# Optimization experiments

Hardware: AMD Instinct MI355X
Metric: run time of the kernel (lower is better)

Reference implementation:

```python
import jax, jax.numpy as jnp
import numpy as np

EPS = 1e-9
NUM_HEADS = 16
D = 1024      # input_dim == hidden_dim
B, S = 2, 2048


def layer_norm(x, scale, shift):
    mu = x.mean(axis=-1, keepdims=True)
    # torch std is unbiased (ddof=1); eps added to std, not variance
    std = jnp.std(x, axis=-1, ddof=1, keepdims=True)
    return scale * (x - mu) / (std + EPS) + shift


def setup_inputs() -> dict:
    key = jax.random.key(0)
    ks = jax.random.split(key, 18)
    d, h = D, D
    w = lambda k, sh: jax.random.normal(k, sh, dtype=jnp.float32) * 0.02
    return {
        "inputs": jax.random.normal(ks[0], (B, S, d), dtype=jnp.float32),
        "ln1_scale": jax.random.normal(ks[1], (d,), dtype=jnp.float32),
        "ln1_shift": jax.random.normal(ks[2], (d,), dtype=jnp.float32),
        "Wq": w(ks[3], (d, h)), "bq": jnp.zeros((h,), jnp.float32),
        "Wk": w(ks[4], (d, h)), "bk": jnp.zeros((h,), jnp.float32),
        "Wv": w(ks[5], (d, h)), "bv": jnp.zeros((h,), jnp.float32),
        "Wo": w(ks[6], (h, d)), "bo": jnp.zeros((d,), jnp.float32),
        "W1": w(ks[7], (d, 4 * d)), "b1": jnp.zeros((4 * d,), jnp.float32),
        "W2": w(ks[8], (4 * d, d)), "b2": jnp.zeros((d,), jnp.float32),
        "ln2_scale": jax.random.normal(ks[9], (d,), dtype=jnp.float32),
        "ln2_shift": jax.random.normal(ks[10], (d,), dtype=jnp.float32),
    }


def mhsa(x, Wq, bq, Wk, bk, Wv, bv, Wo, bo):
    b, s, d = x.shape
    nh, dh = NUM_HEADS, D // NUM_HEADS
    q = (x @ Wq + bq).reshape(b, s, nh, dh).transpose(0, 2, 1, 3)  # b h s d
    k = (x @ Wk + bk).reshape(b, s, nh, dh).transpose(0, 2, 1, 3)
    v = (x @ Wv + bv).reshape(b, s, nh, dh).transpose(0, 2, 1, 3)
    scores = jnp.einsum("bhqd,bhkd->bhqk", q, k) / jnp.sqrt(jnp.float32(dh))
    causal = jnp.triu(jnp.ones((s, s), dtype=bool), k=1)  # mask above diagonal
    scores = jnp.where(causal, -jnp.inf, scores)
    p = jax.nn.softmax(scores, axis=-1)
    p = jnp.where(jnp.isnan(p), 0.0, p)  # NaN-fill as in original
    out = jnp.einsum("bhqk,bhkd->bhqd", p, v)
    out = out.transpose(0, 2, 1, 3).reshape(b, s, nh * dh)
    return out @ Wo + bo


def reference(inputs, ln1_scale, ln1_shift, Wq, bq, Wk, bk, Wv, bv, Wo, bo,
              W1, b1, W2, b2, ln2_scale, ln2_shift):
    o1 = layer_norm(inputs, ln1_scale, ln1_shift)
    o1 = mhsa(o1, Wq, bq, Wk, bk, Wv, bv, Wo, bo) + inputs
    o2 = layer_norm(o1, ln2_scale, ln2_shift)
    # NOTE: original adds the residual from the *normalized* tensor, not o1
    ffn = jax.nn.relu(o2 @ W1 + b1) @ W2 + b2
    return ffn + o2
```

## Files before the change

### kernel.cpp

```cpp
#include <hip/hip_runtime.h>
#include <hip/hip_bf16.h>
#include <math.h>

#define BB 2
#define SS 2048
#define DD 1024
#define HH 16
#define DH 64
#define NROW (BB*SS)
#define FFN (4*DD)

typedef __attribute__((ext_vector_type(8))) __bf16 bf16x8;
typedef __attribute__((ext_vector_type(4))) float f32x4;

__device__ __forceinline__ ushort f2b(float f) {
    union { float f; uint32_t u; } x; x.f = f;
    uint32_t r = x.u + 0x7FFF + ((x.u >> 16) & 1);
    return (ushort)(r >> 16);
}
__device__ __forceinline__ float b2f(ushort u) {
    union { uint32_t u; float f; } x; x.u = (uint32_t)u << 16;
    return x.f;
}

__global__ __launch_bounds__(256)
void ln_kernel(const float* __restrict__ x, const float* __restrict__ scale,
               const float* __restrict__ shift, ushort* __restrict__ y) {
    int row = blockIdx.x;
    const float* xr = x + (size_t)row * DD;
    ushort* yr = y + (size_t)row * DD;
    int t = threadIdx.x;
    float v[4];
    float s = 0.f, ss = 0.f;
#pragma unroll
    for (int i = 0; i < 4; ++i) {
        v[i] = xr[t + 256 * i];
        s += v[i];
        ss += v[i] * v[i];
    }
#pragma unroll
    for (int off = 32; off; off >>= 1) {
        s  += __shfl_xor(s, off);
        ss += __shfl_xor(ss, off);
    }
    __shared__ float red[8];
    int w = t >> 6;
    if ((t & 63) == 0) { red[w] = s; red[w + 4] = ss; }
    __syncthreads();
    float st  = red[0] + red[1] + red[2] + red[3];
    float sst = red[4] + red[5] + red[6] + red[7];
    float mu = st * (1.f / DD);
    float var = (sst - DD * mu * mu) * (1.f / (DD - 1));
    var = fmaxf(var, 0.f);
    float inv = 1.f / (sqrtf(var) + 1e-9f);
#pragma unroll
    for (int i = 0; i < 4; ++i) {
        int c = t + 256 * i;
        yr[c] = f2b(scale[c] * (v[i] - mu) * inv + shift[c]);
    }
}

__global__ __launch_bounds__(256)
void ln_res_kernel(const ushort* __restrict__ xa, const float* __restrict__ xb,
                   const float* __restrict__ scale, const float* __restrict__ shift,
                   ushort* __restrict__ yb) {
    int row = blockIdx.x;
    const ushort* ar = xa + (size_t)row * DD;
    const float* br = xb + (size_t)row * DD;
    ushort* ybr = yb + (size_t)row * DD;
    int t = threadIdx.x;
    float v[4];
    float s = 0.f, ss = 0.f;
#pragma unroll
    for (int i = 0; i < 4; ++i) {
        int c = t + 256 * i;
        v[i] = b2f(ar[c]) + br[c];
        s += v[i];
        ss += v[i] * v[i];
    }
#pragma unroll
    for (int off = 32; off; off >>= 1) {
        s  += __shfl_xor(s, off);
        ss += __shfl_xor(ss, off);
    }
    __shared__ float red[8];
    int w = t >> 6;
    if ((t & 63) == 0) { red[w] = s; red[w + 4] = ss; }
    __syncthreads();
    float st  = red[0] + red[1] + red[2] + red[3];
    float sst = red[4] + red[5] + red[6] + red[7];
    float mu = st * (1.f / DD);
    float var = (sst - DD * mu * mu) * (1.f / (DD - 1));
    var = fmaxf(var, 0.f);
    float inv = 1.f / (sqrtf(var) + 1e-9f);
#pragma unroll
    for (int i = 0; i < 4; ++i) {
        int c = t + 256 * i;
        ybr[c] = f2b(scale[c] * (v[i] - mu) * inv + shift[c]);
    }
}

__global__ __launch_bounds__(256)
void transpose_bf16_kernel(const float* __restrict__ W, ushort* __restrict__ Wt,
                           int K, int N) {
    __shared__ ushort tile[32][33];
    int tx = threadIdx.x & 31;
    int ty = threadIdx.x >> 5;
    int n0 = blockIdx.x * 32;
    int k0 = blockIdx.y * 32;
#pragma unroll
    for (int i = 0; i < 32; i += 8)
        tile[ty + i][tx] = f2b(W[(size_t)(k0 + ty + i) * N + n0 + tx]);
    __syncthreads();
#pragma unroll
    for (int i = 0; i < 32; i += 8)
        Wt[(size_t)(n0 + ty + i) * K + k0 + tx] = tile[tx][ty + i];
}

#define GBM 128
#define GBN 128
#define GBK 32

template <int MODE, bool BF16_OUT, int DEPTH>
__global__ __launch_bounds__(512)
void gemm_bf16_kernel(const ushort* __restrict__ A, const ushort* __restrict__ Wt,
                      const float* __restrict__ bias, const ushort* __restrict__ addsrc,
                      void* __restrict__ Cout, int M, int N, int K,
                      const float* __restrict__ bias2, const float* __restrict__ bias3,
                      void* __restrict__ out2, void* __restrict__ out3) {
    __shared__ ushort As[DEPTH][GBM * GBK];
    __shared__ ushort Bs[DEPTH][GBN * GBK];

    int tid = threadIdx.x;
    int lane = tid & 63;
    int wid = tid >> 6;
    int wr = wid >> 2, wc = wid & 3;

    int gx = gridDim.x;
    int nwg = gx * gridDim.y;
    int orig = blockIdx.y * gx + blockIdx.x;
    int q8 = nwg >> 3;
    int swz = (orig & 7) * q8 + (orig >> 3);
    int bx = swz % gx, by = swz / gx;

    int brow = by * GBM;
    int bcol = bx * GBN;

    int lrow = lane & 15;
    int kgrp = lane >> 4;

    f32x4 acc[4][2] = {};

    int srow = tid >> 2;
    int sgran = (tid & 3) ^ ((srow >> 1) & 3);

    auto stage = [&](int buf, int k0) {
        const char* ga = (const char*)A +
            ((size_t)(brow + srow) * K + k0) * 2 + sgran * 16;
        __builtin_amdgcn_global_load_lds(
            (const __attribute__((address_space(1))) uint32_t*)ga,
            (__attribute__((address_space(3))) uint32_t*)(&As[buf][0] + (wid * 16) * GBK),
            16, 0, 0);
        const char* gb = (const char*)Wt +
            ((size_t)(bcol + srow) * K + k0) * 2 + sgran * 16;
        __builtin_amdgcn_global_load_lds(
            (const __attribute__((address_space(1))) uint32_t*)gb,
            (__attribute__((address_space(3))) uint32_t*)(&Bs[buf][0] + (wid * 16) * GBK),
            16, 0, 0);
    };

    int nk = K / GBK;
    constexpr int PRE = DEPTH - 1;
#pragma unroll
    for (int s = 0; s < PRE; ++s)
        if (s < nk) stage(s, s * GBK);

    int cur = 0, stg = PRE;
    for (int t = 0; t < nk; ++t) {
        __builtin_amdgcn_sched_barrier(0);
        int rem = nk - 1 - t;
        if constexpr (DEPTH == 5) {
            if (rem >= 3)      asm volatile("s_waitcnt vmcnt(6)" ::: "memory");
            else if (rem == 2) asm volatile("s_waitcnt vmcnt(4)" ::: "memory");
            else if (rem == 1) asm volatile("s_waitcnt vmcnt(2)" ::: "memory");
            else               asm volatile("s_waitcnt vmcnt(0)" ::: "memory");
        } else {
            if (rem >= 1)      asm volatile("s_waitcnt vmcnt(2)" ::: "memory");
            else               asm volatile("s_waitcnt vmcnt(0)" ::: "memory");
        }
        asm volatile("s_barrier" ::: "memory");
        if (t + PRE < nk) stage(stg, (t + PRE) * GBK);

        bf16x8 afrag[4], bfrag[2];
#pragma unroll
        for (int mi = 0; mi < 4; ++mi) {
            int row = wr * 64 + mi * 16 + lrow;
            int gran = kgrp ^ ((row >> 1) & 3);
            afrag[mi] = *(const bf16x8*)((const char*)&As[cur][0] + row * 64 + gran * 16);
        }
#pragma unroll
        for (int ni = 0; ni < 2; ++ni) {
            int row = wc * 32 + ni * 16 + lrow;
            int gran = kgrp ^ ((row >> 1) & 3);
            bfrag[ni] = *(const bf16x8*)((const char*)&Bs[cur][0] + row * 64 + gran * 16);
        }
#pragma unroll
        for (int mi = 0; mi < 4; ++mi)
#pragma unroll
            for (int ni = 0; ni < 2; ++ni)
                acc[mi][ni] = __builtin_amdgcn_mfma_f32_16x16x32_bf16(
                    afrag[mi], bfrag[ni], acc[mi][ni], 0, 0, 0);

        cur = (cur == DEPTH - 1) ? 0 : cur + 1;
        stg = (stg == DEPTH - 1) ? 0 : stg + 1;
    }

    if (MODE == 3) {
        int which = bcol >> 10;
        const float* bs = which == 0 ? bias : (which == 1 ? bias2 : bias3);
#pragma unroll
        for (int ni = 0; ni < 2; ++ni) {
            int col = bcol + wc * 32 + ni * 16 + lrow;
            int lcol = col & 1023;
            float bsv = bs[lcol];
#pragma unroll
            for (int mi = 0; mi < 4; ++mi) {
                f32x4 a = acc[mi][ni];
#pragma unroll
                for (int j = 0; j < 4; ++j) {
                    int row = brow + wr * 64 + mi * 16 + kgrp * 4 + j;
                    float val = a[j] + bsv;
                    if (which == 2) {
                        size_t idx = (size_t)(row >> 11) * ((size_t)DD * SS)
                                   + (size_t)lcol * SS + (row & (SS - 1));
                        ((ushort*)out3)[idx] = f2b(val);
                    } else {
                        ushort* dst = which == 0 ? (ushort*)Cout : (ushort*)out2;
                        dst[(size_t)row * DD + lcol] = f2b(val);
                    }
                }
            }
        }
        return;
    }

#pragma unroll
    for (int ni = 0; ni < 2; ++ni) {
        int col = bcol + wc * 32 + ni * 16 + lrow;
        float bsv = bias[col];
#pragma unroll
        for (int mi = 0; mi < 4; ++mi) {
            f32x4 a = acc[mi][ni];
#pragma unroll
            for (int j = 0; j < 4; ++j) {
                int row = brow + wr * 64 + mi * 16 + kgrp * 4 + j;
                float val = a[j] + bsv;
                if (MODE == 1) val = fmaxf(val, 0.f);
                if (MODE == 2) val += b2f(addsrc[(size_t)row * N + col]);
                if (BF16_OUT)
                    ((ushort*)Cout)[(size_t)row * N + col] = f2b(val);
                else
                    ((float*)Cout)[(size_t)row * N + col] = val;
            }
        }
    }
}

__global__ __launch_bounds__(256)
void attn_mfma_kernel(const ushort* __restrict__ Qg, const ushort* __restrict__ Kg,
                      const ushort* __restrict__ Vtg, ushort* __restrict__ Og) {
    __shared__ ushort Qs[64 * 64];
    __shared__ ushort Ks[3][64 * 64];
    __shared__ ushort Vs[3][64 * 64];
    __shared__ ushort Ps[64 * 64];

    int tid = threadIdx.x;
    int lane = tid & 63;
    int wid = tid >> 6;
    int bh = blockIdx.x;
    int b = bh >> 4, h = bh & 15;
    int q0 = ((int)gridDim.y - 1 - (int)blockIdx.y) * 64;

    const ushort* Qbase = Qg + ((size_t)(b * SS + q0)) * DD + h * DH;
    const ushort* Kbase = Kg + ((size_t)(b * SS)) * DD + h * DH;
    const ushort* Vbase = Vtg + (size_t)bh * DH * SS;

    int r0 = wid * 16;
    int rr0 = r0 + (lane >> 3);
    int g0 = lane & 7;

    auto stageKV = [&](int buf, int k0) {
#pragma unroll
        for (int i = 0; i < 2; ++i) {
            int rr = rr0 + i * 8;
            int g = g0 ^ (rr & 7);
            const ushort* srck = Kbase + (size_t)(k0 + rr) * DD + g * 8;
            __builtin_amdgcn_global_load_lds(
                (const __attribute__((address_space(1))) uint32_t*)srck,
                (__attribute__((address_space(3))) uint32_t*)(&Ks[buf][0] + (r0 + i * 8) * 64),
                16, 0, 0);
            const ushort* srcv = Vbase + (size_t)rr * SS + k0 + g * 8;
            __builtin_amdgcn_global_load_lds(
                (const __attribute__((address_space(1))) uint32_t*)srcv,
                (__attribute__((address_space(3))) uint32_t*)(&Vs[buf][0] + (r0 + i * 8) * 64),
                16, 0, 0);
        }
    };

    int nt = q0 / 64 + 1;

    {
#pragma unroll
        for (int i = 0; i < 2; ++i) {
            int rr = rr0 + i * 8;
            int g = g0 ^ (rr & 7);
            const ushort* src = Qbase + (size_t)rr * DD + g * 8;
            __builtin_amdgcn_global_load_lds(
                (const __attribute__((address_space(1))) uint32_t*)src,
                (__attribute__((address_space(3))) uint32_t*)(Qs + (r0 + i * 8) * 64),
                16, 0, 0);
        }
    }
    stageKV(0, 0);
    if (nt > 1) stageKV(1, 64);
    __builtin_amdgcn_sched_barrier(0);
    if (nt > 1) asm volatile("s_waitcnt vmcnt(8)" ::: "memory");
    else        asm volatile("s_waitcnt vmcnt(4)" ::: "memory");
    asm volatile("s_barrier" ::: "memory");

    bf16x8 aq[2];
    {
        int r = wid * 16 + (lane & 15);
#pragma unroll
        for (int ks = 0; ks < 2; ++ks) {
            int lg = ks * 4 + (lane >> 4);
            aq[ks] = *(const bf16x8*)((const char*)Qs + r * 128 + ((lg ^ (r & 7)) << 4));
        }
    }

    f32x4 oacc[4] = {};
    float m[4] = {-INFINITY, -INFINITY, -INFINITY, -INFINITY};
    float l[4] = {0.f, 0.f, 0.f, 0.f};

    int cur = 0, stg = 2;
    for (int t = 0; t < nt; ++t) {
        __builtin_amdgcn_sched_barrier(0);
        if (t + 1 < nt) asm volatile("s_waitcnt vmcnt(4)" ::: "memory");
        else            asm volatile("s_waitcnt vmcnt(0)" ::: "memory");
        asm volatile("s_barrier" ::: "memory");
        if (t + 2 < nt) stageKV(stg, (t + 2) * 64);
        int k0 = t * 64;

        f32x4 sacc[4] = {};
#pragma unroll
        for (int ni = 0; ni < 4; ++ni) {
            int r = ni * 16 + (lane & 15);
#pragma unroll
            for (int ks = 0; ks < 2; ++ks) {
                int lg = ks * 4 + (lane >> 4);
                bf16x8 bk = *(const bf16x8*)((const char*)&Ks[cur][0] + r * 128 + ((lg ^ (r & 7)) << 4));
                sacc[ni] = __builtin_amdgcn_mfma_f32_16x16x32_bf16(aq[ks], bk, sacc[ni], 0, 0, 0);
            }
        }

        float sc[4][4];
#pragma unroll
        for (int ni = 0; ni < 4; ++ni)
#pragma unroll
            for (int j = 0; j < 4; ++j)
                sc[ni][j] = sacc[ni][j] * 0.125f;
        if (k0 == q0) {
            int rl = wid * 16 + ((lane >> 4) << 2);
#pragma unroll
            for (int ni = 0; ni < 4; ++ni) {
                int key = ni * 16 + (lane & 15);
#pragma unroll
                for (int j = 0; j < 4; ++j)
                    if (key > rl + j) sc[ni][j] = -INFINITY;
            }
        }

        float p[4][4];
#pragma unroll
        for (int j = 0; j < 4; ++j) {
            float mx = fmaxf(fmaxf(sc[0][j], sc[1][j]), fmaxf(sc[2][j], sc[3][j]));
#pragma unroll
            for (int off = 1; off < 16; off <<= 1) mx = fmaxf(mx, __shfl_xor(mx, off));
            float mn = fmaxf(m[j], mx);
            float corr = __expf(m[j] - mn);
            m[j] = mn;
            float rs = 0.f;
#pragma unroll
            for (int ni = 0; ni < 4; ++ni) { p[ni][j] = __expf(sc[ni][j] - mn); rs += p[ni][j]; }
#pragma unroll
            for (int off = 1; off < 16; off <<= 1) rs += __shfl_xor(rs, off);
            l[j] = l[j] * corr + rs;
#pragma unroll
            for (int ni = 0; ni < 4; ++ni) oacc[ni][j] *= corr;
        }

        {
            int rbase = wid * 16 + ((lane >> 4) << 2);
            int cl = lane & 15;
#pragma unroll
            for (int ni = 0; ni < 4; ++ni) {
                int c = ni * 16 + cl;
                int gsh = (c >> 3);
                int blo = (c & 7) * 2;
#pragma unroll
                for (int j = 0; j < 4; ++j) {
                    int rl = rbase + j;
                    *(ushort*)((char*)Ps + rl * 128 + ((gsh ^ (rl & 7)) << 4) + blo) = f2b(p[ni][j]);
                }
            }
        }
        asm volatile("s_waitcnt lgkmcnt(0)" ::: "memory");

        bf16x8 ap[2];
        {
            int r = wid * 16 + (lane & 15);
#pragma unroll
            for (int ks = 0; ks < 2; ++ks) {
                int lg = ks * 4 + (lane >> 4);
                ap[ks] = *(const bf16x8*)((const char*)Ps + r * 128 + ((lg ^ (r & 7)) << 4));
            }
        }
#pragma unroll
        for (int ni = 0; ni < 4; ++ni) {
            int r = ni * 16 + (lane & 15);
#pragma unroll
            for (int ks = 0; ks < 2; ++ks) {
                int lg = ks * 4 + (lane >> 4);
                bf16x8 bv = *(const bf16x8*)((const char*)&Vs[cur][0] + r * 128 + ((lg ^ (r & 7)) << 4));
                oacc[ni] = __builtin_amdgcn_mfma_f32_16x16x32_bf16(ap[ks], bv, oacc[ni], 0, 0, 0);
            }
        }
        cur = (cur == 2) ? 0 : cur + 1;
        stg = (stg == 2) ? 0 : stg + 1;
    }

#pragma unroll
    for (int j = 0; j < 4; ++j) {
        float inv = 1.f / l[j];
        int gr = q0 + wid * 16 + ((lane >> 4) << 2) + j;
#pragma unroll
        for (int ni = 0; ni < 4; ++ni) {
            int d = ni * 16 + (lane & 15);
            Og[((size_t)(b * SS + gr)) * DD + h * DH + d] = f2b(oacc[ni][j] * inv);
        }
    }
}

extern "C" void kernel_launch(void* const* d_in, const int* in_sizes, int n_in,
                              void* d_out, int out_size, void* d_ws, size_t ws_size,
                              hipStream_t stream) {
    const float* inputs    = (const float*)d_in[0];
    const float* ln1_scale = (const float*)d_in[1];
    const float* ln1_shift = (const float*)d_in[2];
    const float* Wq = (const float*)d_in[3];
    const float* bq = (const float*)d_in[4];
    const float* Wk = (const float*)d_in[5];
    const float* bk = (const float*)d_in[6];
    const float* Wv = (const float*)d_in[7];
    const float* bv = (const float*)d_in[8];
    const float* Wo = (const float*)d_in[9];
    const float* bo = (const float*)d_in[10];
    const float* W1 = (const float*)d_in[11];
    const float* b1 = (const float*)d_in[12];
    const float* W2 = (const float*)d_in[13];
    const float* b2 = (const float*)d_in[14];
    const float* ln2_scale = (const float*)d_in[15];
    const float* ln2_shift = (const float*)d_in[16];
    float* out = (float*)d_out;

    const size_t MB = 1024 * 1024;
    char* w = (char*)d_ws;
    ushort* q_b   = (ushort*)(w + 0 * MB);
    ushort* k_b   = (ushort*)(w + 8 * MB);
    ushort* vt_b  = (ushort*)(w + 16 * MB);
    ushort* att_b = (ushort*)(w + 24 * MB);
    ushort* proj_b= (ushort*)(w + 32 * MB);
    ushort* o2_b  = (ushort*)(w + 48 * MB);
    ushort* h1_b  = (ushort*)(w + 64 * MB);
    ushort* wq_t  = (ushort*)(w + 96 * MB);
    ushort* wk_t  = (ushort*)(w + 98 * MB);
    ushort* wv_t  = (ushort*)(w + 100 * MB);
    ushort* wo_t  = (ushort*)(w + 102 * MB);
    ushort* w1_t  = (ushort*)(w + 104 * MB);
    ushort* w2_t  = (ushort*)(w + 112 * MB);
    ushort* xn_b  = (ushort*)(w + 120 * MB);

    transpose_bf16_kernel<<<dim3(DD / 32, DD / 32), 256, 0, stream>>>(Wq, wq_t, DD, DD);
    transpose_bf16_kernel<<<dim3(DD / 32, DD / 32), 256, 0, stream>>>(Wk, wk_t, DD, DD);
    transpose_bf16_kernel<<<dim3(DD / 32, DD / 32), 256, 0, stream>>>(Wv, wv_t, DD, DD);
    transpose_bf16_kernel<<<dim3(DD / 32, DD / 32), 256, 0, stream>>>(Wo, wo_t, DD, DD);
    transpose_bf16_kernel<<<dim3(FFN / 32, DD / 32), 256, 0, stream>>>(W1, w1_t, DD, FFN);
    transpose_bf16_kernel<<<dim3(DD / 32, FFN / 32), 256, 0, stream>>>(W2, w2_t, FFN, DD);

    ln_kernel<<<NROW, 256, 0, stream>>>(inputs, ln1_scale, ln1_shift, xn_b);

    dim3 gqkv(3 * DD / GBN, NROW / GBM);
    gemm_bf16_kernel<3, true, 3><<<gqkv, 512, 0, stream>>>(
        xn_b, wq_t, bq, nullptr, q_b, NROW, 3 * DD, DD, bk, bv, k_b, vt_b);

    dim3 ga(BB * HH, SS / 64);
    attn_mfma_kernel<<<ga, 256, 0, stream>>>(q_b, k_b, vt_b, att_b);

    dim3 g1(DD / GBN, NROW / GBM);
    gemm_bf16_kernel<0, true, 5><<<g1, 512, 0, stream>>>(
        att_b, wo_t, bo, nullptr, proj_b, NROW, DD, DD, nullptr, nullptr, nullptr, nullptr);

    ln_res_kernel<<<NROW, 256, 0, stream>>>(proj_b, inputs, ln2_scale, ln2_shift, o2_b);

    dim3 g2(FFN / GBN, NROW / GBM);
    gemm_bf16_kernel<1, true, 3><<<g2, 512, 0, stream>>>(
        o2_b, w1_t, b1, nullptr, h1_b, NROW, FFN, DD, nullptr, nullptr, nullptr, nullptr);

    gemm_bf16_kernel<2, false, 5><<<g1, 512, 0, stream>>>(
        h1_b, w2_t, b2, o2_b, out, NROW, DD, FFN, nullptr, nullptr, nullptr, nullptr);
}
```

Before: 283.3 us.

## Transpose score MFMA so each lane owns one query row in attention softmax

```diff
diff --git a/kernel.cpp b/kernel.cpp
--- a/kernel.cpp
+++ b/kernel.cpp
@@ -270,9 +270,8 @@
 void attn_mfma_kernel(const ushort* __restrict__ Qg, const ushort* __restrict__ Kg,
                       const ushort* __restrict__ Vtg, ushort* __restrict__ Og) {
     __shared__ ushort Qs[64 * 64];
-    __shared__ ushort Ks[3][64 * 64];
-    __shared__ ushort Vs[3][64 * 64];
-    __shared__ ushort Ps[64 * 64];
+    __shared__ ushort Ks[2][64 * 64];
+    __shared__ ushort Vs[2][64 * 64];
 
     int tid = threadIdx.x;
     int lane = tid & 63;
@@ -288,18 +287,20 @@
     int r0 = wid * 16;
     int rr0 = r0 + (lane >> 3);
     int g0 = lane & 7;
+    int g = lane >> 4;
+    int lr = lane & 15;
 
     auto stageKV = [&](int buf, int k0) {
 #pragma unroll
         for (int i = 0; i < 2; ++i) {
             int rr = rr0 + i * 8;
-            int g = g0 ^ (rr & 7);
-            const ushort* srck = Kbase + (size_t)(k0 + rr) * DD + g * 8;
+            int gg = g0 ^ (rr & 7);
+            const ushort* srck = Kbase + (size_t)(k0 + rr) * DD + gg * 8;
             __builtin_amdgcn_global_load_lds(
                 (const __attribute__((address_space(1))) uint32_t*)srck,
                 (__attribute__((address_space(3))) uint32_t*)(&Ks[buf][0] + (r0 + i * 8) * 64),
                 16, 0, 0);
-            const ushort* srcv = Vbase + (size_t)rr * SS + k0 + g * 8;
+            const ushort* srcv = Vbase + (size_t)rr * SS + k0 + gg * 8;
             __builtin_amdgcn_global_load_lds(
                 (const __attribute__((address_space(1))) uint32_t*)srcv,
                 (__attribute__((address_space(3))) uint32_t*)(&Vs[buf][0] + (r0 + i * 8) * 64),
@@ -313,8 +314,8 @@
 #pragma unroll
         for (int i = 0; i < 2; ++i) {
             int rr = rr0 + i * 8;
-            int g = g0 ^ (rr & 7);
-            const ushort* src = Qbase + (size_t)rr * DD + g * 8;
+            int gg = g0 ^ (rr & 7);
+            const ushort* src = Qbase + (size_t)rr * DD + gg * 8;
             __builtin_amdgcn_global_load_lds(
                 (const __attribute__((address_space(1))) uint32_t*)src,
                 (__attribute__((address_space(3))) uint32_t*)(Qs + (r0 + i * 8) * 64),
@@ -322,46 +323,44 @@
         }
     }
     stageKV(0, 0);
-    if (nt > 1) stageKV(1, 64);
-    __builtin_amdgcn_sched_barrier(0);
-    if (nt > 1) asm volatile("s_waitcnt vmcnt(8)" ::: "memory");
-    else        asm volatile("s_waitcnt vmcnt(4)" ::: "memory");
-    asm volatile("s_barrier" ::: "memory");
+    asm volatile("s_waitcnt vmcnt(4)" ::: "memory");
 
     bf16x8 aq[2];
     {
-        int r = wid * 16 + (lane & 15);
+        int r = wid * 16 + lr;
 #pragma unroll
         for (int ks = 0; ks < 2; ++ks) {
-            int lg = ks * 4 + (lane >> 4);
+            int lg = ks * 4 + g;
             aq[ks] = *(const bf16x8*)((const char*)Qs + r * 128 + ((lg ^ (r & 7)) << 4));
         }
     }
+    ushort* Ps = Qs;
 
     f32x4 oacc[4] = {};
-    float m[4] = {-INFINITY, -INFINITY, -INFINITY, -INFINITY};
-    float l[4] = {0.f, 0.f, 0.f, 0.f};
-
-    int cur = 0, stg = 2;
+    float m = -INFINITY, l = 0.f;
+    int qa = q0 + wid * 16 + lr;
+
+    int cur = 0;
     for (int t = 0; t < nt; ++t) {
         __builtin_amdgcn_sched_barrier(0);
-        if (t + 1 < nt) asm volatile("s_waitcnt vmcnt(4)" ::: "memory");
-        else            asm volatile("s_waitcnt vmcnt(0)" ::: "memory");
+        asm volatile("s_waitcnt vmcnt(0)" ::: "memory");
         asm volatile("s_barrier" ::: "memory");
-        if (t + 2 < nt) stageKV(stg, (t + 2) * 64);
+        if (t + 1 < nt) stageKV(cur ^ 1, (t + 1) * 64);
         int k0 = t * 64;
 
         f32x4 sacc[4] = {};
+        __builtin_amdgcn_s_setprio(1);
 #pragma unroll
         for (int ni = 0; ni < 4; ++ni) {
-            int r = ni * 16 + (lane & 15);
+            int r = ni * 16 + lr;
 #pragma unroll
             for (int ks = 0; ks < 2; ++ks) {
-                int lg = ks * 4 + (lane >> 4);
+                int lg = ks * 4 + g;
                 bf16x8 bk = *(const bf16x8*)((const char*)&Ks[cur][0] + r * 128 + ((lg ^ (r & 7)) << 4));
-                sacc[ni] = __builtin_amdgcn_mfma_f32_16x16x32_bf16(aq[ks], bk, sacc[ni], 0, 0, 0);
-            }
-        }
+                sacc[ni] = __builtin_amdgcn_mfma_f32_16x16x32_bf16(bk, aq[ks], sacc[ni], 0, 0, 0);
+            }
+        }
+        __builtin_amdgcn_s_setprio(0);
 
         float sc[4][4];
 #pragma unroll
@@ -370,82 +369,90 @@
             for (int j = 0; j < 4; ++j)
                 sc[ni][j] = sacc[ni][j] * 0.125f;
         if (k0 == q0) {
-            int rl = wid * 16 + ((lane >> 4) << 2);
 #pragma unroll
             for (int ni = 0; ni < 4; ++ni) {
-                int key = ni * 16 + (lane & 15);
-#pragma unroll
-                for (int j = 0; j < 4; ++j)
-                    if (key > rl + j) sc[ni][j] = -INFINITY;
-            }
-        }
-
+#pragma unroll
+                for (int j = 0; j < 4; ++j) {
+                    int key = q0 + ni * 16 + g * 4 + j;
+                    if (key > qa) sc[ni][j] = -INFINITY;
+                }
+            }
+        }
+
+        float mx = sc[0][0];
+#pragma unroll
+        for (int ni = 0; ni < 4; ++ni)
+#pragma unroll
+            for (int j = 0; j < 4; ++j) mx = fmaxf(mx, sc[ni][j]);
+        mx = fmaxf(mx, __shfl_xor(mx, 16));
+        mx = fmaxf(mx, __shfl_xor(mx, 32));
+        float mn = fmaxf(m, mx);
+        float corr = __expf(m - mn);
+        m = mn;
         float p[4][4];
-#pragma unroll
-        for (int j = 0; j < 4; ++j) {
-            float mx = fmaxf(fmaxf(sc[0][j], sc[1][j]), fmaxf(sc[2][j], sc[3][j]));
-#pragma unroll
-            for (int off = 1; off < 16; off <<= 1) mx = fmaxf(mx, __shfl_xor(mx, off));
-            float mn = fmaxf(m[j], mx);
-            float corr = __expf(m[j] - mn);
-            m[j] = mn;
-            float rs = 0.f;
-#pragma unroll
-            for (int ni = 0; ni < 4; ++ni) { p[ni][j] = __expf(sc[ni][j] - mn); rs += p[ni][j]; }
-#pragma unroll
-            for (int off = 1; off < 16; off <<= 1) rs += __shfl_xor(rs, off);
-            l[j] = l[j] * corr + rs;
-#pragma unroll
-            for (int ni = 0; ni < 4; ++ni) oacc[ni][j] *= corr;
-        }
+        float rs = 0.f;
+#pragma unroll
+        for (int ni = 0; ni < 4; ++ni)
+#pragma unroll
+            for (int j = 0; j < 4; ++j) { p[ni][j] = __expf(sc[ni][j] - mn); rs += p[ni][j]; }
+        rs += __shfl_xor(rs, 16);
+        rs += __shfl_xor(rs, 32);
+        l = l * corr + rs;
+
+        float cj[4];
+#pragma unroll
+        for (int j = 0; j < 4; ++j)
+            cj[j] = __shfl(corr, (lane & 48) | (g * 4 + j));
+#pragma unroll
+        for (int ni = 0; ni < 4; ++ni)
+#pragma unroll
+            for (int j = 0; j < 4; ++j) oacc[ni][j] *= cj[j];
 
         {
-            int rbase = wid * 16 + ((lane >> 4) << 2);
-            int cl = lane & 15;
+            int row = wid * 16 + lr;
 #pragma unroll
             for (int ni = 0; ni < 4; ++ni) {
-                int c = ni * 16 + cl;
-                int gsh = (c >> 3);
-                int blo = (c & 7) * 2;
-#pragma unroll
-                for (int j = 0; j < 4; ++j) {
-                    int rl = rbase + j;
-                    *(ushort*)((char*)Ps + rl * 128 + ((gsh ^ (rl & 7)) << 4) + blo) = f2b(p[ni][j]);
-                }
+                ushort4 w4;
+                w4.x = f2b(p[ni][0]); w4.y = f2b(p[ni][1]);
+                w4.z = f2b(p[ni][2]); w4.w = f2b(p[ni][3]);
+                int gran = (ni * 2 + (g >> 1)) ^ (row & 7);
+                *(ushort4*)((char*)Ps + row * 128 + (gran << 4) + (g & 1) * 8) = w4;
             }
         }
         asm volatile("s_waitcnt lgkmcnt(0)" ::: "memory");
 
         bf16x8 ap[2];
         {
-            int r = wid * 16 + (lane & 15);
+            int r = wid * 16 + lr;
 #pragma unroll
             for (int ks = 0; ks < 2; ++ks) {
-                int lg = ks * 4 + (lane >> 4);
+                int lg = ks * 4 + g;
                 ap[ks] = *(const bf16x8*)((const char*)Ps + r * 128 + ((lg ^ (r & 7)) << 4));
             }
         }
+        __builtin_amdgcn_s_setprio(1);
 #pragma unroll
         for (int ni = 0; ni < 4; ++ni) {
-            int r = ni * 16 + (lane & 15);
+            int r = ni * 16 + lr;
 #pragma unroll
             for (int ks = 0; ks < 2; ++ks) {
-                int lg = ks * 4 + (lane >> 4);
+                int lg = ks * 4 + g;
                 bf16x8 bv = *(const bf16x8*)((const char*)&Vs[cur][0] + r * 128 + ((lg ^ (r & 7)) << 4));
                 oacc[ni] = __builtin_amdgcn_mfma_f32_16x16x32_bf16(ap[ks], bv, oacc[ni], 0, 0, 0);
             }
         }
-        cur = (cur == 2) ? 0 : cur + 1;
-        stg = (stg == 2) ? 0 : stg + 1;
+        __builtin_amdgcn_s_setprio(0);
+        cur ^= 1;
     }
 
 #pragma unroll
     for (int j = 0; j < 4; ++j) {
-        float inv = 1.f / l[j];
-        int gr = q0 + wid * 16 + ((lane >> 4) << 2) + j;
+        float lj = __shfl(l, (lane & 48) | (g * 4 + j));
+        float inv = 1.f / lj;
+        int gr = q0 + wid * 16 + g * 4 + j;
 #pragma unroll
         for (int ni = 0; ni < 4; ++ni) {
-            int d = ni * 16 + (lane & 15);
+            int d = ni * 16 + lr;
             Og[((size_t)(b * SS + gr)) * DD + h * DH + d] = f2b(oacc[ni][j] * inv);
         }
     }
```

Result: faster. 268.0 us (-5.4%).
